# Kernel tuning notes

Hardware: AMD Instinct MI355X
Metric: run time of the kernel (lower is better)

## Reference

```python
import jax, jax.numpy as jnp
import numpy as np

SP = 4      # sp_size (number of simulated sequence-parallel ranks)
NH = 16     # num_attention_heads
HD = 64     # head_dim
HS = 1024   # hidden_size
B = 1       # batch
S = 8192    # global sequence length (SP chunks of 2048)


def setup_inputs() -> dict:
    key = jax.random.key(0)
    ks = jax.random.split(key, 9)
    w_scale = 1.0 / np.sqrt(HS)
    def w(k):
        # xavier-ish init, stored as [in, out] so y = x @ W + b
        return jax.random.uniform(k, (HS, HS), jnp.float32, -w_scale, w_scale)
    return {
        'hidden_states': jax.random.normal(ks[0], (B, S, HS), jnp.float32),
        'Wq': w(ks[1]), 'bq': jnp.zeros((HS,), jnp.float32),
        'Wk': w(ks[2]), 'bk': jnp.zeros((HS,), jnp.float32),
        'Wv': w(ks[3]), 'bv': jnp.zeros((HS,), jnp.float32),
        'Wo': w(ks[4]), 'bo': jnp.zeros((HS,), jnp.float32),
    }


def reference(hidden_states, Wq, bq, Wk, bk, Wv, bv, Wo, bo):
    b, s, _ = hidden_states.shape
    sc = s // SP  # per-rank chunk length
    inv_sqrt_hd = 1.0 / np.sqrt(HD)

    def heads(x):
        # [B, S, HS] -> [SP, B, NH, Sc, HD]
        return x.reshape(b, SP, sc, NH, HD).transpose(1, 0, 3, 2, 4)

    q = heads(hidden_states @ Wq + bq)
    k = heads(hidden_states @ Wk + bk)
    v = heads(hidden_states @ Wv + bv)

    out = jnp.zeros_like(q)
    # ring attention: at step i each rank r attends to chunk (r + i) mod SP
    for i in range(SP):
        ki = jnp.roll(k, -i, axis=0)
        vi = jnp.roll(v, -i, axis=0)
        scores = jnp.einsum('sbhqd,sbhkd->sbhqk', q, ki) * inv_sqrt_hd
        probs = jax.nn.softmax(scores, axis=-1)  # per-chunk softmax (faithful to source)
        out = out + jnp.einsum('sbhqk,sbhkd->sbhqd', probs, vi)
    out = out / SP  # source divides accumulated context by sp_size

    # [SP, B, NH, Sc, HD] -> [B, S, NH*HD]
    ctx = out.transpose(1, 0, 3, 2, 4).reshape(b, s, NH * HD)
    return ctx @ Wo + bo
```

## Files before the change

kernel.cpp:

```cpp
#include <hip/hip_runtime.h>

#define DEVINL __device__ __forceinline__

typedef __attribute__((ext_vector_type(8))) short short8;
typedef __attribute__((ext_vector_type(4))) float floatx4;
typedef __attribute__((ext_vector_type(4))) unsigned uintx4;
typedef __attribute__((ext_vector_type(2))) unsigned uintx2;

DEVINL unsigned short f2bf(float f){
  unsigned u = __builtin_bit_cast(unsigned, f);
  u += 0x7FFFu + ((u >> 16) & 1u);
  return (unsigned short)(u >> 16);
}
DEVINL unsigned pk2(float a, float b){
  unsigned ua = __builtin_bit_cast(unsigned, a);
  unsigned ub = __builtin_bit_cast(unsigned, b);
  ua += 0x7FFFu + ((ua >> 16) & 1u);
  ub += 0x7FFFu + ((ub >> 16) & 1u);
  return (ua >> 16) | (ub & 0xFFFF0000u);
}
DEVINL float bf2f(unsigned short h){
  unsigned u = ((unsigned)h) << 16;
  return __builtin_bit_cast(float, u);
}
DEVINL void gload_lds16(const void* g, void* l){
  __builtin_amdgcn_global_load_lds((const __attribute__((address_space(1))) void*)g,
                                   (__attribute__((address_space(3))) void*)l, 16, 0, 0);
}
DEVINL int perm2(int k){
  return (((k >> 4) & 1) << 5) | (((k >> 2) & 3) << 3) | (((k >> 5) & 1) << 2) | (k & 3);
}

__global__ void k_detect(const unsigned* __restrict__ w, int* __restrict__ flag){
  __shared__ int cnt;
  if (threadIdx.x == 0) cnt = 0;
  __syncthreads();
  int c = 0;
  for (int i = threadIdx.x; i < 1024; i += 256){
    unsigned e = (w[i] >> 7) & 0xFFu;
    c += (e >= 120u && e <= 132u) ? 1 : 0;
  }
  atomicAdd(&cnt, c);
  __syncthreads();
  if (threadIdx.x == 0) *flag = (cnt > 512) ? 1 : 0;
}

__global__ void k_conv_bf16(const void* __restrict__ src, unsigned short* __restrict__ dst,
                            int n, const int* __restrict__ flag){
  int i = (blockIdx.x * 256 + threadIdx.x) * 8;
  if (i >= n) return;
  if (*flag){
    ((uint4*)dst)[i >> 3] = ((const uint4*)src)[i >> 3];
  } else {
    const float* s = (const float*)src;
    short8 v;
    #pragma unroll
    for (int j = 0; j < 8; j++) v[j] = (short)f2bf(s[i + j]);
    *(short8*)(dst + i) = v;
  }
}

__global__ void k_conv_wT(const void* __restrict__ src, unsigned short* __restrict__ dst,
                          const int* __restrict__ flag){
  __shared__ float tile[32][33];
  const int tx = threadIdx.x & 31, ty = threadIdx.x >> 5;
  const int bx = blockIdx.x, by = blockIdx.y;
  const int isbf = *flag;
  #pragma unroll
  for (int r = 0; r < 32; r += 8){
    int k = by*32 + ty + r, n = bx*32 + tx;
    float v = isbf ? bf2f(((const unsigned short*)src)[k*1024 + n])
                   : ((const float*)src)[k*1024 + n];
    tile[ty + r][tx] = v;
  }
  __syncthreads();
  #pragma unroll
  for (int r = 0; r < 32; r += 8){
    int n = bx*32 + ty + r, k = by*32 + tx;
    dst[n*1024 + k] = f2bf(tile[tx][ty + r]);
  }
}

__global__ void k_conv_f32(const void* __restrict__ src, float* __restrict__ dst,
                           int n, const int* __restrict__ flag){
  int i = blockIdx.x * 256 + threadIdx.x;
  if (i >= n) return;
  dst[i] = (*flag) ? bf2f(((const unsigned short*)src)[i]) : ((const float*)src)[i];
}

template<int MODE>
__global__ __launch_bounds__(256, 2) void k_gemm(
    const unsigned short* __restrict__ A, const unsigned short* __restrict__ Bt,
    const float* __restrict__ bias, void* __restrict__ Cout, const int* __restrict__ flagp,
    float scale)
{
  const int K = 1024;
  __shared__ __align__(16) unsigned short As[128*32];
  __shared__ __align__(16) unsigned short Bs[128*32];
  const int tid = threadIdx.x;
  const int lane = tid & 63, wave = tid >> 6;
  const int quad = lane >> 4, l15 = lane & 15;
  const int m0 = blockIdx.x * 128, n0 = blockIdx.y * 128;
  const int wm = (wave >> 1) * 64, wn = (wave & 1) * 64;
  const floatx4 fzero = {0.f, 0.f, 0.f, 0.f};
  floatx4 acc[4][4];
  #pragma unroll
  for (int i = 0; i < 4; i++)
    #pragma unroll
    for (int j = 0; j < 4; j++) acc[i][j] = fzero;

  for (int k0 = 0; k0 < K; k0 += 32){
    __syncthreads();
    #pragma unroll
    for (int rep = 0; rep < 2; rep++){
      int idx = tid + rep*256;
      int row = idx >> 2, c = idx & 3;
      gload_lds16(A  + (size_t)(m0 + row)*K + (k0 + c*8), &As[idx*8]);
      gload_lds16(Bt + (size_t)(n0 + row)*K + (k0 + c*8), &Bs[idx*8]);
    }
    asm volatile("s_waitcnt vmcnt(0)" ::: "memory");
    __syncthreads();
    short8 af[4], bf[4];
    #pragma unroll
    for (int i = 0; i < 4; i++) af[i] = *(const short8*)&As[(wm + i*16 + l15)*32 + quad*8];
    #pragma unroll
    for (int j = 0; j < 4; j++) bf[j] = *(const short8*)&Bs[(wn + j*16 + l15)*32 + quad*8];
    #pragma unroll
    for (int i = 0; i < 4; i++)
      #pragma unroll
      for (int j = 0; j < 4; j++)
        acc[i][j] = __builtin_amdgcn_mfma_f32_16x16x32_bf16(af[i], bf[j], acc[i][j], 0, 0, 0);
  }

  float bs[4];
  #pragma unroll
  for (int j = 0; j < 4; j++) bs[j] = bias[n0 + wn + j*16 + l15];
  const int useBf = (MODE == 1) ? *flagp : 1;
  #pragma unroll
  for (int i = 0; i < 4; i++){
    #pragma unroll
    for (int j = 0; j < 4; j++){
      int n = n0 + wn + j*16 + l15;
      #pragma unroll
      for (int r = 0; r < 4; r++){
        int m = m0 + wm + i*16 + quad*4 + r;
        float v = (acc[i][j][r] + bs[j]) * scale;
        if (MODE == 0){
          ((unsigned short*)Cout)[((size_t)(n >> 6)*8192 + m)*64 + (n & 63)] = f2bf(v);
        } else if (MODE == 2){
          ((unsigned short*)Cout)[(size_t)n*8192 + ((m & ~63) | perm2(m & 63))] = f2bf(v);
        } else {
          if (useBf) ((unsigned short*)Cout)[(size_t)m*1024 + n] = f2bf(v);
          else       ((float*)Cout)[(size_t)m*1024 + n] = v;
        }
      }
    }
  }
}

__global__ __launch_bounds__(256, 3) void k_attn(
    const unsigned short* __restrict__ Qg, const unsigned short* __restrict__ Kg,
    const unsigned short* __restrict__ Vg, unsigned short* __restrict__ ctx)
{
  __shared__ __align__(16) unsigned short Qs[128*72];
  __shared__ __align__(16) unsigned short Ks[64*72];
  __shared__ __align__(16) unsigned short Vs[64*72];
  const int tid = threadIdx.x, lane = tid & 63, wave = tid >> 6;
  const int quad = lane >> 4, l15 = lane & 15;
  const int bid = blockIdx.x;
  const int xcd = bid & 7, slot = bid >> 3;
  const int h = xcd*2 + (slot >> 6);
  const int rem = slot & 63, rchunk = rem >> 4, qt = rem & 15;
  const int sq0 = rchunk*2048 + qt*128;
  const unsigned short* Qh = Qg + (size_t)h*8192*64;
  const unsigned short* Kh = Kg + (size_t)h*8192*64;
  const unsigned short* Vh = Vg + (size_t)h*8192*64;
  const int wm = wave * 32;
  const floatx4 fzero = {0.f, 0.f, 0.f, 0.f};

  #pragma unroll
  for (int rep = 0; rep < 4; rep++){
    int idx = tid + rep*256, row = idx >> 3, c = idx & 7;
    short8 v = *(const short8*)(Qh + (size_t)(sq0 + row)*64 + c*8);
    *(short8*)&Qs[row*72 + c*8] = v;
  }
  __syncthreads();
  short8 qf[2][2];
  #pragma unroll
  for (int mi = 0; mi < 2; mi++)
    #pragma unroll
    for (int ks = 0; ks < 2; ks++)
      qf[mi][ks] = *(const short8*)&Qs[(wm + mi*16 + l15)*72 + ks*32 + quad*8];

  floatx4 Of[2][4];
  #pragma unroll
  for (int mi = 0; mi < 2; mi++)
    #pragma unroll
    for (int di = 0; di < 4; di++) Of[mi][di] = fzero;

  short8 tk[2], tv[2];
  {
    int kvs = (rchunk & 3)*2048;
    #pragma unroll
    for (int rep = 0; rep < 2; rep++){
      int idx = tid + rep*256, row = idx >> 3, c = idx & 7;
      tk[rep] = *(const short8*)(Kh + (size_t)(kvs + row)*64 + c*8);
      tv[rep] = *(const short8*)(Vh + (size_t)row*8192 + kvs + c*8);
    }
  }

  for (int i = 0; i < 4; i++){
    float lacc[2] = {0.f, 0.f};
    floatx4 Oc[2][4];
    #pragma unroll
    for (int mi = 0; mi < 2; mi++)
      #pragma unroll
      for (int di = 0; di < 4; di++) Oc[mi][di] = fzero;

    for (int kt = 0; kt < 32; kt++){
      __syncthreads();
      #pragma unroll
      for (int rep = 0; rep < 2; rep++){
        int idx = tid + rep*256, row = idx >> 3, c = idx & 7;
        *(short8*)&Ks[row*72 + c*8] = tk[rep];
        *(short8*)&Vs[row*72 + c*8] = tv[rep];
      }
      {
        int lin = i*32 + kt + 1;
        int ni2 = (lin >> 5) & 3, nkt = lin & 31;
        int nkvs = ((rchunk + ni2) & 3)*2048 + nkt*64;
        #pragma unroll
        for (int rep = 0; rep < 2; rep++){
          int idx = tid + rep*256, row = idx >> 3, c = idx & 7;
          tk[rep] = *(const short8*)(Kh + (size_t)(nkvs + row)*64 + c*8);
          tv[rep] = *(const short8*)(Vh + (size_t)row*8192 + nkvs + c*8);
        }
      }
      __syncthreads();

      floatx4 St[2][4];
      #pragma unroll
      for (int mi = 0; mi < 2; mi++)
        #pragma unroll
        for (int ni = 0; ni < 4; ni++) St[mi][ni] = fzero;
      #pragma unroll
      for (int ks = 0; ks < 2; ks++)
        #pragma unroll
        for (int ni = 0; ni < 4; ni++){
          short8 kf = *(const short8*)&Ks[(ni*16 + l15)*72 + ks*32 + quad*8];
          #pragma unroll
          for (int mi = 0; mi < 2; mi++)
            St[mi][ni] = __builtin_amdgcn_mfma_f32_16x16x32_bf16(kf, qf[mi][ks], St[mi][ni], 0, 0, 0);
        }

      short8 pf[2][2];
      #pragma unroll
      for (int mi = 0; mi < 2; mi++){
        float e[4][4];
        float part = 0.f;
        #pragma unroll
        for (int ni = 0; ni < 4; ni++)
          #pragma unroll
          for (int r = 0; r < 4; r++){
            e[ni][r] = __builtin_amdgcn_exp2f(St[mi][ni][r]);
            part += e[ni][r];
          }
        lacc[mi] += part;
        #pragma unroll
        for (int ks = 0; ks < 2; ks++){
          uintx4 w;
          w[0] = pk2(e[ks  ][0], e[ks  ][1]);
          w[1] = pk2(e[ks  ][2], e[ks  ][3]);
          w[2] = pk2(e[2+ks][0], e[2+ks][1]);
          w[3] = pk2(e[2+ks][2], e[2+ks][3]);
          pf[mi][ks] = __builtin_bit_cast(short8, w);
        }
      }

      #pragma unroll
      for (int ks = 0; ks < 2; ks++)
        #pragma unroll
        for (int di = 0; di < 4; di++){
          short8 vf = *(const short8*)&Vs[(di*16 + l15)*72 + ks*32 + quad*8];
          #pragma unroll
          for (int mi = 0; mi < 2; mi++)
            Oc[mi][di] = __builtin_amdgcn_mfma_f32_16x16x32_bf16(vf, pf[mi][ks], Oc[mi][di], 0, 0, 0);
        }
    }

    #pragma unroll
    for (int mi = 0; mi < 2; mi++){
      float ls = lacc[mi];
      ls += __shfl_xor(ls, 16);
      ls += __shfl_xor(ls, 32);
      float inv = __builtin_amdgcn_rcpf(ls);
      #pragma unroll
      for (int di = 0; di < 4; di++)
        #pragma unroll
        for (int r = 0; r < 4; r++) Of[mi][di][r] += Oc[mi][di][r] * inv;
    }
  }

  #pragma unroll
  for (int mi = 0; mi < 2; mi++){
    int q = sq0 + wm + mi*16 + l15;
    #pragma unroll
    for (int di = 0; di < 4; di++){
      uintx2 w;
      w[0] = pk2(Of[mi][di][0]*0.25f, Of[mi][di][1]*0.25f);
      w[1] = pk2(Of[mi][di][2]*0.25f, Of[mi][di][3]*0.25f);
      *(uintx2*)&ctx[(size_t)q*1024 + h*64 + di*16 + quad*4] = w;
    }
  }
}

extern "C" void kernel_launch(void* const* d_in, const int* in_sizes, int n_in,
                              void* d_out, int out_size, void* d_ws, size_t ws_size,
                              hipStream_t stream)
{
  (void)in_sizes; (void)n_in; (void)out_size; (void)ws_size;
  char* ws = (char*)d_ws;
  size_t off = 0;
  auto alloc = [&](size_t bytes) -> char* {
    char* p = ws + off;
    off = (off + bytes + 255) & ~(size_t)255;
    return p;
  };
  int* flag            = (int*)alloc(4);
  unsigned short* hsb  = (unsigned short*)alloc((size_t)8192*1024*2);
  unsigned short* wqt  = (unsigned short*)alloc((size_t)1024*1024*2);
  unsigned short* wkt  = (unsigned short*)alloc((size_t)1024*1024*2);
  unsigned short* wvt  = (unsigned short*)alloc((size_t)1024*1024*2);
  unsigned short* wot  = (unsigned short*)alloc((size_t)1024*1024*2);
  float* bqf           = (float*)alloc(1024*4);
  float* bkf           = (float*)alloc(1024*4);
  float* bvf           = (float*)alloc(1024*4);
  float* bof           = (float*)alloc(1024*4);
  unsigned short* Qb   = (unsigned short*)alloc((size_t)16*8192*64*2);
  unsigned short* Kb   = (unsigned short*)alloc((size_t)16*8192*64*2);
  unsigned short* Vb   = (unsigned short*)alloc((size_t)16*8192*64*2);
  unsigned short* ctxb = (unsigned short*)alloc((size_t)8192*1024*2);

  k_detect<<<1, 256, 0, stream>>>((const unsigned*)d_in[0], flag);
  k_conv_bf16<<<4096, 256, 0, stream>>>(d_in[0], hsb, 8192*1024, flag);
  k_conv_wT<<<dim3(32,32), 256, 0, stream>>>(d_in[1], wqt, flag);
  k_conv_wT<<<dim3(32,32), 256, 0, stream>>>(d_in[3], wkt, flag);
  k_conv_wT<<<dim3(32,32), 256, 0, stream>>>(d_in[5], wvt, flag);
  k_conv_wT<<<dim3(32,32), 256, 0, stream>>>(d_in[7], wot, flag);
  k_conv_f32<<<4, 256, 0, stream>>>(d_in[2], bqf, 1024, flag);
  k_conv_f32<<<4, 256, 0, stream>>>(d_in[4], bkf, 1024, flag);
  k_conv_f32<<<4, 256, 0, stream>>>(d_in[6], bvf, 1024, flag);
  k_conv_f32<<<4, 256, 0, stream>>>(d_in[8], bof, 1024, flag);

  const float Cs = 0.18033688011112042f;
  dim3 gg(64, 8);
  k_gemm<0><<<gg, 256, 0, stream>>>(hsb, wqt, bqf, Qb, nullptr, Cs);
  k_gemm<0><<<gg, 256, 0, stream>>>(hsb, wkt, bkf, Kb, nullptr, 1.0f);
  k_gemm<2><<<gg, 256, 0, stream>>>(hsb, wvt, bvf, Vb, nullptr, 1.0f);

  k_attn<<<1024, 256, 0, stream>>>(Qb, Kb, Vb, ctxb);

  k_gemm<1><<<gg, 256, 0, stream>>>(ctxb, wot, bof, d_out, flag, 1.0f);
}
```

Measured before the change: 576.9 us.

## Fuse QKV GEMMs and enlarge attention Q tile with double-buffered swizzled LDS

The three Q/K/V projection GEMMs become one launch with a 3x wider N grid that routes each output column block to the Q, K or V buffer. This relies on the transposed weights and biases sitting contiguously in the workspace. The attention kernel now handles 256 query rows per block (64 per wave) so each K/V tile is reused by twice as many queries. It double-buffers K/V in XOR-swizzled, unpadded LDS, which removes one barrier per iteration. A cheaper round-half-up bf16 packing of the probabilities replaces the round-to-nearest-even packing, at the cost of a small precision difference and more registers per wave.

After: 521.1 us. 9.7% less time.

```diff
diff --git a/kernel.cpp b/kernel.cpp
--- a/kernel.cpp
+++ b/kernel.cpp
@@ -4,7 +4,6 @@
 
 typedef __attribute__((ext_vector_type(8))) short short8;
 typedef __attribute__((ext_vector_type(4))) float floatx4;
-typedef __attribute__((ext_vector_type(4))) unsigned uintx4;
 typedef __attribute__((ext_vector_type(2))) unsigned uintx2;
 
 DEVINL unsigned short f2bf(float f){
@@ -18,6 +17,11 @@
   ua += 0x7FFFu + ((ua >> 16) & 1u);
   ub += 0x7FFFu + ((ub >> 16) & 1u);
   return (ua >> 16) | (ub & 0xFFFF0000u);
+}
+DEVINL unsigned pkfast(float a, float b){
+  unsigned ua = __builtin_bit_cast(unsigned, a) + 0x8000u;
+  unsigned ub = __builtin_bit_cast(unsigned, b) + 0x8000u;
+  return __builtin_amdgcn_perm(ub, ua, 0x07060302u);
 }
 DEVINL float bf2f(unsigned short h){
   unsigned u = ((unsigned)h) << 16;
@@ -91,8 +95,8 @@
 template<int MODE>
 __global__ __launch_bounds__(256, 2) void k_gemm(
     const unsigned short* __restrict__ A, const unsigned short* __restrict__ Bt,
-    const float* __restrict__ bias, void* __restrict__ Cout, const int* __restrict__ flagp,
-    float scale)
+    const float* __restrict__ bias, void* __restrict__ C0, void* __restrict__ C1,
+    void* __restrict__ C2, const int* __restrict__ flagp, float scale)
 {
   const int K = 1024;
   __shared__ __align__(16) unsigned short As[128*32];
@@ -144,136 +148,140 @@
       #pragma unroll
       for (int r = 0; r < 4; r++){
         int m = m0 + wm + i*16 + quad*4 + r;
-        float v = (acc[i][j][r] + bs[j]) * scale;
-        if (MODE == 0){
-          ((unsigned short*)Cout)[((size_t)(n >> 6)*8192 + m)*64 + (n & 63)] = f2bf(v);
-        } else if (MODE == 2){
-          ((unsigned short*)Cout)[(size_t)n*8192 + ((m & ~63) | perm2(m & 63))] = f2bf(v);
+        float v = acc[i][j][r] + bs[j];
+        if (MODE == 3){
+          int sel = n >> 10, nn = n & 1023;
+          if (sel == 0){
+            ((unsigned short*)C0)[((size_t)(nn >> 6)*8192 + m)*64 + (nn & 63)] = f2bf(v * scale);
+          } else if (sel == 1){
+            ((unsigned short*)C1)[((size_t)(nn >> 6)*8192 + m)*64 + (nn & 63)] = f2bf(v);
+          } else {
+            ((unsigned short*)C2)[(size_t)nn*8192 + ((m & ~63) | perm2(m & 63))] = f2bf(v);
+          }
         } else {
-          if (useBf) ((unsigned short*)Cout)[(size_t)m*1024 + n] = f2bf(v);
-          else       ((float*)Cout)[(size_t)m*1024 + n] = v;
+          if (useBf) ((unsigned short*)C0)[(size_t)m*1024 + n] = f2bf(v);
+          else       ((float*)C0)[(size_t)m*1024 + n] = v;
         }
       }
     }
   }
 }
 
-__global__ __launch_bounds__(256, 3) void k_attn(
+__global__ __launch_bounds__(256, 2) void k_attn(
     const unsigned short* __restrict__ Qg, const unsigned short* __restrict__ Kg,
     const unsigned short* __restrict__ Vg, unsigned short* __restrict__ ctx)
 {
-  __shared__ __align__(16) unsigned short Qs[128*72];
-  __shared__ __align__(16) unsigned short Ks[64*72];
-  __shared__ __align__(16) unsigned short Vs[64*72];
+  __shared__ __align__(16) unsigned short Qs[256*64];
+  __shared__ __align__(16) unsigned short Ks[2][64*64];
+  __shared__ __align__(16) unsigned short Vs[2][64*64];
   const int tid = threadIdx.x, lane = tid & 63, wave = tid >> 6;
   const int quad = lane >> 4, l15 = lane & 15;
   const int bid = blockIdx.x;
   const int xcd = bid & 7, slot = bid >> 3;
-  const int h = xcd*2 + (slot >> 6);
-  const int rem = slot & 63, rchunk = rem >> 4, qt = rem & 15;
-  const int sq0 = rchunk*2048 + qt*128;
+  const int h = xcd*2 + (slot >> 5);
+  const int rem = slot & 31, rchunk = rem >> 3, qt = rem & 7;
+  const int sq0 = rchunk*2048 + qt*256;
   const unsigned short* Qh = Qg + (size_t)h*8192*64;
   const unsigned short* Kh = Kg + (size_t)h*8192*64;
   const unsigned short* Vh = Vg + (size_t)h*8192*64;
-  const int wm = wave * 32;
+  const int wq0 = wave * 64;
   const floatx4 fzero = {0.f, 0.f, 0.f, 0.f};
 
   #pragma unroll
-  for (int rep = 0; rep < 4; rep++){
+  for (int rep = 0; rep < 8; rep++){
     int idx = tid + rep*256, row = idx >> 3, c = idx & 7;
     short8 v = *(const short8*)(Qh + (size_t)(sq0 + row)*64 + c*8);
-    *(short8*)&Qs[row*72 + c*8] = v;
+    *(short8*)&Qs[row*64 + (c ^ (row & 7))*8] = v;
   }
   __syncthreads();
-  short8 qf[2][2];
-  #pragma unroll
-  for (int mi = 0; mi < 2; mi++)
-    #pragma unroll
-    for (int ks = 0; ks < 2; ks++)
-      qf[mi][ks] = *(const short8*)&Qs[(wm + mi*16 + l15)*72 + ks*32 + quad*8];
-
-  floatx4 Of[2][4];
-  #pragma unroll
-  for (int mi = 0; mi < 2; mi++)
-    #pragma unroll
-    for (int di = 0; di < 4; di++) Of[mi][di] = fzero;
+  short8 qf[4][2];
+  #pragma unroll
+  for (int mi = 0; mi < 4; mi++)
+    #pragma unroll
+    for (int ks = 0; ks < 2; ks++){
+      int row = wq0 + mi*16 + l15;
+      qf[mi][ks] = *(const short8*)&Qs[row*64 + (((ks*4 + quad) ^ (row & 7)))*8];
+    }
 
   short8 tk[2], tv[2];
-  {
-    int kvs = (rchunk & 3)*2048;
+  auto loadKV = [&](int t){
+    int ci = (t >> 5) & 3;
+    int kvs = ((rchunk + ci) & 3)*2048 + (t & 31)*64;
     #pragma unroll
     for (int rep = 0; rep < 2; rep++){
       int idx = tid + rep*256, row = idx >> 3, c = idx & 7;
       tk[rep] = *(const short8*)(Kh + (size_t)(kvs + row)*64 + c*8);
       tv[rep] = *(const short8*)(Vh + (size_t)row*8192 + kvs + c*8);
     }
-  }
+  };
+  auto storeKV = [&](int buf){
+    #pragma unroll
+    for (int rep = 0; rep < 2; rep++){
+      int idx = tid + rep*256, row = idx >> 3, c = idx & 7;
+      int pos = row*64 + (c ^ (row & 7))*8;
+      *(short8*)&Ks[buf][pos] = tk[rep];
+      *(short8*)&Vs[buf][pos] = tv[rep];
+    }
+  };
+
+  loadKV(0);
+  storeKV(0);
+
+  floatx4 Of[4][4];
+  #pragma unroll
+  for (int mi = 0; mi < 4; mi++)
+    #pragma unroll
+    for (int di = 0; di < 4; di++) Of[mi][di] = fzero;
 
   for (int i = 0; i < 4; i++){
-    float lacc[2] = {0.f, 0.f};
-    floatx4 Oc[2][4];
-    #pragma unroll
-    for (int mi = 0; mi < 2; mi++)
+    float lacc[4] = {0.f, 0.f, 0.f, 0.f};
+    floatx4 Oc[4][4];
+    #pragma unroll
+    for (int mi = 0; mi < 4; mi++)
       #pragma unroll
       for (int di = 0; di < 4; di++) Oc[mi][di] = fzero;
 
     for (int kt = 0; kt < 32; kt++){
+      const int t = i*32 + kt, cur = t & 1;
       __syncthreads();
-      #pragma unroll
-      for (int rep = 0; rep < 2; rep++){
-        int idx = tid + rep*256, row = idx >> 3, c = idx & 7;
-        *(short8*)&Ks[row*72 + c*8] = tk[rep];
-        *(short8*)&Vs[row*72 + c*8] = tv[rep];
+      {
+        int nt = (t + 1 < 128) ? (t + 1) : 127;
+        loadKV(nt);
       }
-      {
-        int lin = i*32 + kt + 1;
-        int ni2 = (lin >> 5) & 3, nkt = lin & 31;
-        int nkvs = ((rchunk + ni2) & 3)*2048 + nkt*64;
-        #pragma unroll
-        for (int rep = 0; rep < 2; rep++){
-          int idx = tid + rep*256, row = idx >> 3, c = idx & 7;
-          tk[rep] = *(const short8*)(Kh + (size_t)(nkvs + row)*64 + c*8);
-          tv[rep] = *(const short8*)(Vh + (size_t)row*8192 + nkvs + c*8);
-        }
-      }
-      __syncthreads();
-
-      floatx4 St[2][4];
-      #pragma unroll
-      for (int mi = 0; mi < 2; mi++)
-        #pragma unroll
-        for (int ni = 0; ni < 4; ni++) St[mi][ni] = fzero;
-      #pragma unroll
-      for (int ks = 0; ks < 2; ks++)
-        #pragma unroll
-        for (int ni = 0; ni < 4; ni++){
-          short8 kf = *(const short8*)&Ks[(ni*16 + l15)*72 + ks*32 + quad*8];
+
+      short8 pf[4][2];
+      #pragma unroll
+      for (int mi = 0; mi < 4; mi++){
+        floatx4 St[4];
+        #pragma unroll
+        for (int ni = 0; ni < 4; ni++) St[ni] = fzero;
+        #pragma unroll
+        for (int ks = 0; ks < 2; ks++)
           #pragma unroll
-          for (int mi = 0; mi < 2; mi++)
-            St[mi][ni] = __builtin_amdgcn_mfma_f32_16x16x32_bf16(kf, qf[mi][ks], St[mi][ni], 0, 0, 0);
-        }
-
-      short8 pf[2][2];
-      #pragma unroll
-      for (int mi = 0; mi < 2; mi++){
-        float e[4][4];
+          for (int ni = 0; ni < 4; ni++){
+            int krow = ni*16 + l15;
+            short8 kf = *(const short8*)&Ks[cur][krow*64 + (((ks*4 + quad) ^ (krow & 7)))*8];
+            St[ni] = __builtin_amdgcn_mfma_f32_16x16x32_bf16(kf, qf[mi][ks], St[ni], 0, 0, 0);
+          }
         float part = 0.f;
         #pragma unroll
         for (int ni = 0; ni < 4; ni++)
           #pragma unroll
           for (int r = 0; r < 4; r++){
-            e[ni][r] = __builtin_amdgcn_exp2f(St[mi][ni][r]);
-            part += e[ni][r];
+            St[ni][r] = __builtin_amdgcn_exp2f(St[ni][r]);
+            part += St[ni][r];
           }
         lacc[mi] += part;
         #pragma unroll
         for (int ks = 0; ks < 2; ks++){
-          uintx4 w;
-          w[0] = pk2(e[ks  ][0], e[ks  ][1]);
-          w[1] = pk2(e[ks  ][2], e[ks  ][3]);
-          w[2] = pk2(e[2+ks][0], e[2+ks][1]);
-          w[3] = pk2(e[2+ks][2], e[2+ks][3]);
-          pf[mi][ks] = __builtin_bit_cast(short8, w);
+          uintx2 lo, hi;
+          lo[0] = pkfast(St[ks  ][0], St[ks  ][1]);
+          lo[1] = pkfast(St[ks  ][2], St[ks  ][3]);
+          hi[0] = pkfast(St[2+ks][0], St[2+ks][1]);
+          hi[1] = pkfast(St[2+ks][2], St[2+ks][3]);
+          union { uintx2 u[2]; short8 s; } cv;
+          cv.u[0] = lo; cv.u[1] = hi;
+          pf[mi][ks] = cv.s;
         }
       }
 
@@ -281,15 +289,18 @@
       for (int ks = 0; ks < 2; ks++)
         #pragma unroll
         for (int di = 0; di < 4; di++){
-          short8 vf = *(const short8*)&Vs[(di*16 + l15)*72 + ks*32 + quad*8];
+          int vrow = di*16 + l15;
+          short8 vf = *(const short8*)&Vs[cur][vrow*64 + (((ks*4 + quad) ^ (vrow & 7)))*8];
           #pragma unroll
-          for (int mi = 0; mi < 2; mi++)
+          for (int mi = 0; mi < 4; mi++)
             Oc[mi][di] = __builtin_amdgcn_mfma_f32_16x16x32_bf16(vf, pf[mi][ks], Oc[mi][di], 0, 0, 0);
         }
-    }
-
-    #pragma unroll
-    for (int mi = 0; mi < 2; mi++){
+
+      storeKV(cur ^ 1);
+    }
+
+    #pragma unroll
+    for (int mi = 0; mi < 4; mi++){
       float ls = lacc[mi];
       ls += __shfl_xor(ls, 16);
       ls += __shfl_xor(ls, 32);
@@ -302,8 +313,8 @@
   }
 
   #pragma unroll
-  for (int mi = 0; mi < 2; mi++){
-    int q = sq0 + wm + mi*16 + l15;
+  for (int mi = 0; mi < 4; mi++){
+    int q = sq0 + wq0 + mi*16 + l15;
     #pragma unroll
     for (int di = 0; di < 4; di++){
       uintx2 w;
@@ -353,12 +364,9 @@
   k_conv_f32<<<4, 256, 0, stream>>>(d_in[8], bof, 1024, flag);
 
   const float Cs = 0.18033688011112042f;
-  dim3 gg(64, 8);
-  k_gemm<0><<<gg, 256, 0, stream>>>(hsb, wqt, bqf, Qb, nullptr, Cs);
-  k_gemm<0><<<gg, 256, 0, stream>>>(hsb, wkt, bkf, Kb, nullptr, 1.0f);
-  k_gemm<2><<<gg, 256, 0, stream>>>(hsb, wvt, bvf, Vb, nullptr, 1.0f);
-
-  k_attn<<<1024, 256, 0, stream>>>(Qb, Kb, Vb, ctxb);
-
-  k_gemm<1><<<gg, 256, 0, stream>>>(ctxb, wot, bof, d_out, flag, 1.0f);
-}
+  k_gemm<3><<<dim3(64, 24), 256, 0, stream>>>(hsb, wqt, bqf, Qb, Kb, Vb, nullptr, Cs);
+
+  k_attn<<<512, 256, 0, stream>>>(Qb, Kb, Vb, ctxb);
+
+  k_gemm<1><<<dim3(64, 8), 256, 0, stream>>>(ctxb, wot, bof, d_out, nullptr, nullptr, flag, 1.0f);
+}
```
